# Performance work log

Hardware: AMD Instinct MI355X
Metric: run time of the kernel (lower is better)

The kernel has to match this reference:

```python
import jax, jax.numpy as jnp
import numpy as np

HEAD_DIM = 256
V_DIM = 256
HIDDEN = 1024
SCALE_BASE = 512
GAMMA = 0.96875
BATCH, SEQ = 4, 4096


def _dup_interleave(m):
    # (L, d/2) -> (L, d), duplicating each column consecutively
    return jnp.repeat(m, 2, axis=-1)


def _rotate_every_two(x):
    x1 = x[..., ::2]
    x2 = x[..., 1::2]
    return jnp.stack([-x2, x1], axis=-1).reshape(x.shape)


def _xpos(x, downscale=False):
    # x: (B, L, head_dim); offset=0 path of XPOS.forward
    B, L, Dh = x.shape
    half = Dh // 2
    scale_buf = (jnp.arange(0, Dh, 2, dtype=jnp.float32) + 0.4 * Dh) / (1.4 * Dh)  # (half,)
    pos = jnpp = jnp.arange(L, dtype=jnp.float32)
    scale = scale_buf[None, :] ** (pos / SCALE_BASE)[:, None]  # (L, half)
    inv_freq = 1.0 / (10000.0 ** (jnp.arange(half, dtype=jnp.float32) / half))
    sinusoid = pos[:, None] * inv_freq[None, :]  # (L, half)
    sin, cos = jnp.sin(sinusoid), jnp.cos(sinusoid)
    if downscale:
        scale = 1.0 / scale
    cos_s = _dup_interleave(cos * scale)  # (L, Dh)
    sin_s = _dup_interleave(sin * scale)
    return x * cos_s[None] + _rotate_every_two(x) * sin_s[None]


def _decay_matrix(L):
    n = jnp.arange(L)[:, None]
    m = jnp.arange(L)[None, :]
    mask = n >= m
    expo = jnp.where(mask, n - m, 0).astype(jnp.float32)
    return jnp.where(mask, GAMMA ** expo, 0.0)  # (L, L)


def setup_inputs() -> dict:
    key = jax.random.key(0)
    k1, k2, k3, k4 = jax.random.split(key, 4)
    X = jax.random.normal(k1, (BATCH, SEQ, HIDDEN), dtype=jnp.float32)
    W_Q = jax.random.normal(k2, (HIDDEN, HEAD_DIM), dtype=jnp.float32) / HIDDEN
    W_K = jax.random.normal(k3, (HIDDEN, HEAD_DIM), dtype=jnp.float32) / HIDDEN
    W_V = jax.random.normal(k4, (HIDDEN, V_DIM), dtype=jnp.float32) / HIDDEN
    return {"X": X, "W_Q": W_Q, "W_K": W_K, "W_V": W_V}


def reference(X, W_Q, W_K, W_V):
    L = X.shape[1]
    Q = _xpos(X @ W_Q)                      # (B, L, Dh)
    K = _xpos(X @ W_K, downscale=True)      # (B, L, Dh)
    V = X @ W_V                             # (B, L, Dv)
    D = _decay_matrix(L)                    # (L, L)
    ret = jnp.einsum('bqd,bkd->bqk', Q, K) * D[None]  # (B, L, L)
    return ret @ V                          # (B, L, Dv)
```

## Files before the change

### kernel.cpp

```cpp
#include <hip/hip_runtime.h>
#include <hip/hip_bf16.h>
#include <cstdint>
#include <cstddef>

#define L_SEQ 4096
#define BATCH_N 4
#define HID 1024
#define DH 256
#define LOG2_GAMMA (-0.045803689613124953f)

typedef __attribute__((ext_vector_type(8))) short short8;
typedef __attribute__((ext_vector_type(4))) float floatx4;

__device__ __forceinline__ unsigned short f2bf(float f) {
    union { float f; unsigned int u; } v; v.f = f;
    unsigned int r = (v.u + 0x7FFFu + ((v.u >> 16) & 1u)) >> 16;
    return (unsigned short)r;
}

__device__ __forceinline__ void async_copy16(const unsigned short* gsrc,
                                             unsigned short* lds) {
    __builtin_amdgcn_global_load_lds(
        (const __attribute__((address_space(1))) unsigned int*)gsrc,
        (__attribute__((address_space(3))) unsigned int*)lds, 16, 0, 0);
}

__global__ __launch_bounds__(256) void convert_x_kernel(
    const float* __restrict__ X, unsigned short* __restrict__ Xb)
{
    const int i = (blockIdx.x * 256 + threadIdx.x) * 4;
    const float4 v = *(const float4*)&X[i];
    ushort4 p;
    p.x = f2bf(v.x); p.y = f2bf(v.y); p.z = f2bf(v.z); p.w = f2bf(v.w);
    *(ushort4*)&Xb[i] = p;
}

__global__ __launch_bounds__(256) void transpose_w_kernel(
    const float* __restrict__ WQ, const float* __restrict__ WK,
    const float* __restrict__ WV, unsigned short* __restrict__ Wt)
{
    __shared__ float Ts[64][68];
    const int n0 = blockIdx.x * 64;
    const int k0 = blockIdx.y * 64;
    const int seg = n0 >> 8;
    const float* __restrict__ W = (seg == 0) ? WQ : (seg == 1) ? WK : WV;
    const int nl0 = n0 & 255;

    const int t  = threadIdx.x;
    const int r  = t >> 4;
    const int c4 = (t & 15) * 4;
    #pragma unroll
    for (int i = 0; i < 4; ++i) {
        const int kk = r + i * 16;
        const float4 v = *(const float4*)&W[(size_t)(k0 + kk) * DH + nl0 + c4];
        Ts[c4 + 0][kk] = v.x;
        Ts[c4 + 1][kk] = v.y;
        Ts[c4 + 2][kk] = v.z;
        Ts[c4 + 3][kk] = v.w;
    }
    __syncthreads();
    const int rn = t >> 3;
    const int c8 = (t & 7) * 8;
    #pragma unroll
    for (int i = 0; i < 2; ++i) {
        const int rr = rn + i * 32;
        ushort4 p0, p1;
        p0.x = f2bf(Ts[rr][c8 + 0]); p0.y = f2bf(Ts[rr][c8 + 1]);
        p0.z = f2bf(Ts[rr][c8 + 2]); p0.w = f2bf(Ts[rr][c8 + 3]);
        p1.x = f2bf(Ts[rr][c8 + 4]); p1.y = f2bf(Ts[rr][c8 + 5]);
        p1.z = f2bf(Ts[rr][c8 + 6]); p1.w = f2bf(Ts[rr][c8 + 7]);
        unsigned short* dst = &Wt[(size_t)(n0 + rr) * HID + k0 + c8];
        *(ushort4*)dst       = p0;
        *(ushort4*)(dst + 4) = p1;
    }
}

__global__ __launch_bounds__(256) void gemm_qkv_kernel(
    const unsigned short* __restrict__ Wt,
    const unsigned short* __restrict__ Xb,
    unsigned short* __restrict__ Qo,
    unsigned short* __restrict__ Ko,
    unsigned short* __restrict__ VtG)
{
    __shared__ unsigned short Wa[128][32];
    __shared__ unsigned short Xs[128][32];

    const int dblk = blockIdx.x;
    const int xcd  = dblk & 7;
    const int sq   = dblk >> 3;
    const int by   = xcd * 16 + sq / 6;
    const int bx   = sq % 6;

    const int n0 = bx * 128;
    const int p0 = by * 128;
    const int t    = threadIdx.x;
    const int w    = t >> 6;
    const int lane = t & 63;
    const int quad = lane >> 4;
    const int l16  = lane & 15;
    const int wn   = (w & 1) * 64;
    const int wp   = (w >> 1) * 64;

    const int srow = w * 32 + (lane >> 2);
    const int scol = (lane & 3) * 8;

    floatx4 acc[4][4];
    #pragma unroll
    for (int i = 0; i < 4; ++i)
        #pragma unroll
        for (int j = 0; j < 4; ++j) acc[i][j] = (floatx4){0.f, 0.f, 0.f, 0.f};

    for (int k0 = 0; k0 < HID; k0 += 32) {
        __syncthreads();
        #pragma unroll
        for (int is = 0; is < 2; ++is) {
            const unsigned short* ga =
                &Wt[(size_t)(n0 + srow + is * 16) * HID + k0 + scol];
            const unsigned short* gb =
                &Xb[(size_t)(p0 + srow + is * 16) * HID + k0 + scol];
            async_copy16(ga, &Wa[w * 32 + is * 16][0]);
            async_copy16(gb, &Xs[w * 32 + is * 16][0]);
        }
        __syncthreads();

        short8 af[4], bf[4];
        #pragma unroll
        for (int nt = 0; nt < 4; ++nt)
            af[nt] = *(const short8*)&Wa[wn + nt * 16 + l16][quad * 8];
        #pragma unroll
        for (int pt = 0; pt < 4; ++pt)
            bf[pt] = *(const short8*)&Xs[wp + pt * 16 + l16][quad * 8];
        #pragma unroll
        for (int nt = 0; nt < 4; ++nt)
            #pragma unroll
            for (int pt = 0; pt < 4; ++pt)
                acc[nt][pt] = __builtin_amdgcn_mfma_f32_16x16x32_bf16(
                    af[nt], bf[pt], acc[nt][pt], 0, 0, 0);
    }

    const int seg = n0 >> 8;
    #pragma unroll
    for (int nt = 0; nt < 4; ++nt) {
        const int nfeat = n0 + wn + nt * 16 + quad * 4;
        const int d0 = nfeat & 255;
        #pragma unroll
        for (int pt = 0; pt < 4; ++pt) {
            const int pg  = p0 + wp + pt * 16 + l16;
            const int b   = pg >> 12;
            const int pos = pg & (L_SEQ - 1);
            if (seg == 2) {
                #pragma unroll
                for (int g = 0; g < 4; ++g)
                    VtG[(((size_t)(b * 256 + d0 + g)) << 12) + pos] =
                        f2bf(acc[nt][pt][g]);
            } else {
                const float e = (float)pos * (1.0f / 512.0f);
                float res[4];
                #pragma unroll
                for (int h = 0; h < 4; h += 2) {
                    const int d  = d0 + h;
                    const int i2 = d >> 1;
                    const float sb = ((float)d + 102.4f) * (1.0f / 358.4f);
                    float sc = exp2f(log2f(sb) * e);
                    if (seg == 1) sc = 1.0f / sc;
                    const float invf = exp2f(-13.287712379549449f *
                                             ((float)i2 * (1.0f / 128.0f)));
                    float s, c;
                    sincosf((float)pos * invf, &s, &c);
                    const float cs = c * sc, ss = s * sc;
                    const float xe = acc[nt][pt][h], xo = acc[nt][pt][h + 1];
                    res[h]     = xe * cs - xo * ss;
                    res[h + 1] = xo * cs + xe * ss;
                }
                ushort4 pk;
                pk.x = f2bf(res[0]); pk.y = f2bf(res[1]);
                pk.z = f2bf(res[2]); pk.w = f2bf(res[3]);
                unsigned short* orow =
                    ((seg == 0) ? Qo : Ko) + (size_t)pg * DH + d0;
                *(ushort4*)orow = pk;
            }
        }
    }
}

__global__ __launch_bounds__(256) void retention_kernel(
    const unsigned short* __restrict__ Q,
    const unsigned short* __restrict__ K,
    const unsigned short* __restrict__ VtG,
    float* __restrict__ O)
{
    __shared__ short Qs[64][264];
    __shared__ short Ks[32][264];
    __shared__ short Vt[256][40];
    __shared__ short Ss[64][40];

    const int dblk = blockIdx.x;
    const int xcd  = dblk & 7;
    const int sq   = dblk >> 3;
    const int qt   = xcd * 8 + (sq & 7);
    const int b    = (sq >> 3) & 3;
    const int z    = sq >> 5;

    const int t  = threadIdx.x;
    const int q0 = qt * 64;

    const int w    = t >> 6;
    const int lane = t & 63;
    const int quad = lane >> 4;
    const int l16  = lane & 15;
    const int w16  = w * 16;

    const size_t rbase = (size_t)b * L_SEQ * DH;
    const size_t vbase = ((size_t)b * DH) << 12;

    int kst = q0 - 512; if (kst < 0) kst = 0;
    const int half32 = ((q0 + 64 - kst) >> 6) << 5;
    const int kbeg = kst + (z ? half32 : 0);
    const int kfin = z ? (q0 + 64) : (kst + half32);

    {
        const unsigned short* src = Q + rbase + (size_t)q0 * DH;
        #pragma unroll
        for (int i = 0; i < 8; ++i) {
            const int row = i * 8 + (t >> 5);
            const int col = (t & 31) * 8;
            *(uint4*)&Qs[row][col] = *(const uint4*)&src[row * DH + col];
        }
    }

    floatx4 o[16];
    #pragma unroll
    for (int f = 0; f < 16; ++f) o[f] = (floatx4){0.f, 0.f, 0.f, 0.f};

    for (int k0 = kbeg; k0 < kfin; k0 += 32) {
        __syncthreads();
        {
            const unsigned short* src = K + rbase + (size_t)k0 * DH;
            #pragma unroll
            for (int i = 0; i < 4; ++i) {
                const int row = i * 8 + (t >> 5);
                const int col = (t & 31) * 8;
                *(uint4*)&Ks[row][col] = *(const uint4*)&src[row * DH + col];
            }
        }
        {
            const int c0   = t >> 2;
            const int koff = (t & 3) * 8;
            #pragma unroll
            for (int i = 0; i < 4; ++i) {
                const int c = c0 + 64 * i;
                *(uint4*)&Vt[c][koff] =
                    *(const uint4*)&VtG[vbase + ((size_t)c << 12) + k0 + koff];
            }
        }
        __syncthreads();

        floatx4 s00 = (floatx4){0.f, 0.f, 0.f, 0.f};
        floatx4 s01 = (floatx4){0.f, 0.f, 0.f, 0.f};
        floatx4 s10 = (floatx4){0.f, 0.f, 0.f, 0.f};
        floatx4 s11 = (floatx4){0.f, 0.f, 0.f, 0.f};
        #pragma unroll
        for (int dd = 0; dd < 4; ++dd) {
            const short8 aA  = *(const short8*)&Qs[w16 + l16][dd * 32 + quad * 8];
            const short8 aB  = *(const short8*)&Qs[w16 + l16][(dd + 4) * 32 + quad * 8];
            const short8 b0A = *(const short8*)&Ks[l16][dd * 32 + quad * 8];
            const short8 b1A = *(const short8*)&Ks[16 + l16][dd * 32 + quad * 8];
            const short8 b0B = *(const short8*)&Ks[l16][(dd + 4) * 32 + quad * 8];
            const short8 b1B = *(const short8*)&Ks[16 + l16][(dd + 4) * 32 + quad * 8];
            s00 = __builtin_amdgcn_mfma_f32_16x16x32_bf16(aA, b0A, s00, 0, 0, 0);
            s10 = __builtin_amdgcn_mfma_f32_16x16x32_bf16(aA, b1A, s10, 0, 0, 0);
            s01 = __builtin_amdgcn_mfma_f32_16x16x32_bf16(aB, b0B, s01, 0, 0, 0);
            s11 = __builtin_amdgcn_mfma_f32_16x16x32_bf16(aB, b1B, s11, 0, 0, 0);
        }
        #pragma unroll
        for (int nt = 0; nt < 2; ++nt) {
            const floatx4 sv = nt ? (s10 + s11) : (s00 + s01);
            const int kpos = k0 + nt * 16 + l16;
            #pragma unroll
            for (int g = 0; g < 4; ++g) {
                const int qpos = q0 + w16 + quad * 4 + g;
                const int dq = qpos - kpos;
                const float p = (dq >= 0) ? sv[g] * exp2f((float)dq * LOG2_GAMMA)
                                          : 0.0f;
                Ss[w16 + quad * 4 + g][nt * 16 + l16] = (short)f2bf(p);
            }
        }
        __syncthreads();

        {
            const short8 a = *(const short8*)&Ss[w16 + l16][quad * 8];
            #pragma unroll
            for (int f = 0; f < 16; ++f) {
                const short8 bfr = *(const short8*)&Vt[f * 16 + l16][quad * 8];
                o[f] = __builtin_amdgcn_mfma_f32_16x16x32_bf16(a, bfr, o[f], 0, 0, 0);
            }
        }
    }

    #pragma unroll
    for (int f = 0; f < 16; ++f) {
        #pragma unroll
        for (int g = 0; g < 4; ++g) {
            const int qpos = q0 + w16 + quad * 4 + g;
            atomicAdd(&O[rbase + (size_t)qpos * DH + f * 16 + l16], o[f][g]);
        }
    }
}

extern "C" void kernel_launch(void* const* d_in, const int* in_sizes, int n_in,
                              void* d_out, int out_size, void* d_ws, size_t ws_size,
                              hipStream_t stream)
{
    const float* X  = (const float*)d_in[0];
    const float* WQ = (const float*)d_in[1];
    const float* WK = (const float*)d_in[2];
    const float* WV = (const float*)d_in[3];
    float* out = (float*)d_out;

    const size_t per = (size_t)BATCH_N * L_SEQ * DH;
    unsigned short* Qw  = (unsigned short*)d_ws;
    unsigned short* Kw  = Qw + per;
    unsigned short* Vtw = Kw + per;
    unsigned short* Xbw = Vtw + per;
    unsigned short* Wtw = Xbw + (size_t)16384 * HID;

    hipMemsetAsync(out, 0, per * sizeof(float), stream);

    convert_x_kernel<<<16384, 256, 0, stream>>>(X, Xbw);
    transpose_w_kernel<<<dim3(12, 16), 256, 0, stream>>>(WQ, WK, WV, Wtw);

    gemm_qkv_kernel<<<768, 256, 0, stream>>>(Wtw, Xbw, Qw, Kw, Vtw);

    retention_kernel<<<512, 256, 0, stream>>>(Qw, Kw, Vtw, out);
}
```

Before: 194.1 us.

## Triple-buffer LDS tiles in QKV GEMM with async prefetch two steps ahead

The QKV projection GEMM now keeps three LDS buffers and issues async global-to-LDS copies two k-steps ahead, waiting with vmcnt instead of draining all loads before each tile. The goal is to overlap global memory latency with MFMA work. This triples the LDS footprint of the kernel and depends on hand-written waitcnt values being correct. This GEMM is likely a smaller share of total time than the retention kernel.

```diff
diff --git a/kernel.cpp b/kernel.cpp
--- a/kernel.cpp
+++ b/kernel.cpp
@@ -82,8 +82,8 @@
     unsigned short* __restrict__ Ko,
     unsigned short* __restrict__ VtG)
 {
-    __shared__ unsigned short Wa[128][32];
-    __shared__ unsigned short Xs[128][32];
+    __shared__ unsigned short Wa[3][128][32];
+    __shared__ unsigned short Xs[3][128][32];
 
     const int dblk = blockIdx.x;
     const int xcd  = dblk & 7;
@@ -110,32 +110,47 @@
         #pragma unroll
         for (int j = 0; j < 4; ++j) acc[i][j] = (floatx4){0.f, 0.f, 0.f, 0.f};
 
-    for (int k0 = 0; k0 < HID; k0 += 32) {
-        __syncthreads();
+    const int NT = HID / 32;
+
+    auto stage = [&](int buf, int kt) {
+        const int k0 = kt * 32;
         #pragma unroll
         for (int is = 0; is < 2; ++is) {
             const unsigned short* ga =
                 &Wt[(size_t)(n0 + srow + is * 16) * HID + k0 + scol];
             const unsigned short* gb =
                 &Xb[(size_t)(p0 + srow + is * 16) * HID + k0 + scol];
-            async_copy16(ga, &Wa[w * 32 + is * 16][0]);
-            async_copy16(gb, &Xs[w * 32 + is * 16][0]);
-        }
-        __syncthreads();
-
-        short8 af[4], bf[4];
+            async_copy16(ga, &Wa[buf][w * 32 + is * 16][0]);
+            async_copy16(gb, &Xs[buf][w * 32 + is * 16][0]);
+        }
+    };
+
+    stage(0, 0);
+    stage(1, 1);
+
+    for (int kt = 0; kt < NT; ++kt) {
+        const int buf = kt % 3;
+        if (kt + 1 < NT)
+            asm volatile("s_waitcnt vmcnt(4)" ::: "memory");
+        else
+            asm volatile("s_waitcnt vmcnt(0)" ::: "memory");
+        __builtin_amdgcn_s_barrier();
+
+        if (kt + 2 < NT) stage((kt + 2) % 3, kt + 2);
+
+        short8 af[4], bfv[4];
         #pragma unroll
         for (int nt = 0; nt < 4; ++nt)
-            af[nt] = *(const short8*)&Wa[wn + nt * 16 + l16][quad * 8];
+            af[nt] = *(const short8*)&Wa[buf][wn + nt * 16 + l16][quad * 8];
         #pragma unroll
         for (int pt = 0; pt < 4; ++pt)
-            bf[pt] = *(const short8*)&Xs[wp + pt * 16 + l16][quad * 8];
+            bfv[pt] = *(const short8*)&Xs[buf][wp + pt * 16 + l16][quad * 8];
         #pragma unroll
         for (int nt = 0; nt < 4; ++nt)
             #pragma unroll
             for (int pt = 0; pt < 4; ++pt)
                 acc[nt][pt] = __builtin_amdgcn_mfma_f32_16x16x32_bf16(
-                    af[nt], bf[pt], acc[nt][pt], 0, 0, 0);
+                    af[nt], bfv[pt], acc[nt][pt], 0, 0, 0);
     }
 
     const int seg = n0 >> 8;
```

Result: slower. 201.1 us (+3.6%).
